# Performance work log

Measured on AMD Instinct MI355X. Metric: run time of the kernel, lower is better.

## Reference

```python
import jax, jax.numpy as jnp
import numpy as np

D_MODEL = 768
H = 6
DQK = 128
DV = 256
SCALE_BASE = 512.0


def _xpos(x, sign):
    """xPos rotary: x (B,T,H,d); sign=+1 for queries, -1 for keys."""
    B, T, Hn, d = x.shape
    half = d // 2
    pos = jnp.arange(T, dtype=jnp.float32)
    inv_freq = 1.0 / (10000.0 ** (jnp.arange(half, dtype=jnp.float32) / half))
    angles = pos[:, None] * inv_freq[None, :]                    # (T, half)
    zeta = (jnp.arange(half, dtype=jnp.float32) + half) / d      # (half,)
    decay = zeta[None, :] ** (sign * pos[:, None] / SCALE_BASE)  # (T, half)
    cos_a = (jnp.cos(angles) * decay)[None, :, None, :]
    sin_a = (jnp.sin(angles) * decay)[None, :, None, :]
    x1, x2 = x[..., :half], x[..., half:]
    return jnp.concatenate([x1 * cos_a - x2 * sin_a,
                            x1 * sin_a + x2 * cos_a], axis=-1)


def _decay_mask(T):
    """(H,T,T) causal decay mask, row-normalized by sqrt(row_sum)."""
    gammas = jnp.array([1.0 - 2.0 ** (-(5 + h)) for h in range(H)], dtype=jnp.float32)
    i = jnp.arange(T, dtype=jnp.float32)
    diff = i[:, None] - i[None, :]
    causal = (diff >= 0).astype(jnp.float32)
    D = (gammas[:, None, None] ** jnp.clip(diff, 0.0)[None]) * causal[None]
    row = jnp.clip(jnp.sum(D, axis=-1, keepdims=True), 1e-6)
    return D / jnp.sqrt(row)


def setup_inputs() -> dict:
    key = jax.random.key(0)
    ks = jax.random.split(key, 6)
    B, T = 2, 2048

    def xavier(k, shape):
        lim = float(np.sqrt(6.0 / (shape[0] + shape[1])))
        return jax.random.uniform(k, shape, jnp.float32, -lim, lim)

    return {
        "x": jax.random.normal(ks[0], (B, T, D_MODEL), jnp.float32),
        "Wq": xavier(ks[1], (D_MODEL, H * DQK)),
        "Wk": xavier(ks[2], (D_MODEL, H * DQK)),
        "Wv": xavier(ks[3], (D_MODEL, H * DV)),
        "Wg": xavier(ks[4], (D_MODEL, H * DV)),
        "Wo": xavier(ks[5], (H * DV, D_MODEL)),
        "gn_weight": jnp.ones((H * DV,), jnp.float32),
        "gn_bias": jnp.zeros((H * DV,), jnp.float32),
    }


def reference(x, Wq, Wk, Wv, Wg, Wo, gn_weight, gn_bias):
    B, T, _ = x.shape
    Q = (x @ Wq).reshape(B, T, H, DQK)
    K = (x @ Wk).reshape(B, T, H, DQK)
    V = (x @ Wv).reshape(B, T, H, DV)
    Q = _xpos(Q, 1.0)
    K = _xpos(K, -1.0)
    # retention scores: QK^T * scale * per-head decay mask (no softmax)
    scores = jnp.einsum('bihd,bjhd->bhij', Q, K) * (DQK ** -0.5)
    scores = scores * _decay_mask(T)[None]
    out = jnp.einsum('bhij,bjhv->bihv', scores, V)   # (B,T,H,DV)
    concat = out.reshape(B, T, H * DV)
    # GroupNorm over (channels-in-group, time) per (batch, group), as torch GN on (B,C,T)
    g = concat.transpose(0, 2, 1).reshape(B, H, DV, T)
    mean = jnp.mean(g, axis=(2, 3), keepdims=True)
    var = jnp.var(g, axis=(2, 3), keepdims=True)
    g = (g - mean) / jnp.sqrt(var + 1e-5)
    g = g.reshape(B, H * DV, T) * gn_weight[None, :, None] + gn_bias[None, :, None]
    normed = g.transpose(0, 2, 1)                    # (B,T,H*DV)
    gate = jax.nn.silu(x @ Wg)
    return (normed * gate) @ Wo
```

## Files before the change

### kernel.cpp

```cpp
#include <hip/hip_runtime.h>

typedef unsigned short u16;
typedef unsigned int u32;
typedef __attribute__((ext_vector_type(8))) short short8;
typedef __attribute__((ext_vector_type(4))) float f32x4;

#define DEV static __device__ __forceinline__

DEV float bf2f(u16 u){ u32 i = ((u32)u)<<16; float f; __builtin_memcpy(&f,&i,4); return f; }
DEV u16 f2bf(float f){ u32 i; __builtin_memcpy(&i,&f,4); u32 r = i + 0x7FFFu + ((i>>16)&1u); return (u16)(r>>16); }

DEV void gld16(const void* gp, void* lp){
  __builtin_amdgcn_global_load_lds((const __attribute__((address_space(1))) void*)gp,
                                   (__attribute__((address_space(3))) void*)lp, 16, 0, 0);
}

DEV int bcol(int n, int wc, int ln){ return ((n&1)<<4) + ln + (wc<<5) + ((n>>1)<<6); }

__global__ void k_prep(const float* __restrict__ x,
                       const float* __restrict__ Wq, const float* __restrict__ Wk,
                       const float* __restrict__ Wv, const float* __restrict__ Wg,
                       const float* __restrict__ Wo,
                       u16* __restrict__ xb, u16* __restrict__ WT, u16* __restrict__ WoT,
                       float4* __restrict__ tab){
  __shared__ float tile[32][33];
  int i = blockIdx.x, tid = threadIdx.x;
  if (i < 3072){
    size_t base = ((size_t)i*256 + tid)*4;
    float4 v = *(const float4*)(x + base);
    ushort4 o; o.x=f2bf(v.x); o.y=f2bf(v.y); o.z=f2bf(v.z); o.w=f2bf(v.w);
    *(ushort4*)(xb + base) = o;
  } else if (i < 7680){
    int j = i - 3072;
    const float* src; u16* dst; int N, K, bx, by;
    if (j < 576)       { src=Wq; dst=WT;             N=768;  K=768;  bx=j%24; by=j/24; }
    else if (j < 1152) { int q=j-576;  src=Wk; dst=WT+768ull*768;  N=768;  K=768;  bx=q%24; by=q/24; }
    else if (j < 2304) { int q=j-1152; src=Wv; dst=WT+1536ull*768; N=1536; K=768;  bx=q%48; by=q/48; }
    else if (j < 3456) { int q=j-2304; src=Wg; dst=WT+3072ull*768; N=1536; K=768;  bx=q%48; by=q/48; }
    else               { int q=j-3456; src=Wo; dst=WoT;            N=768;  K=1536; bx=q%24; by=q/24; }
    int n0 = bx*32, k0 = by*32;
    int tx = tid&31, ty = tid>>5;
    #pragma unroll
    for (int q=0;q<4;++q)
      tile[ty + q*8][tx] = src[(size_t)(k0 + ty + q*8)*N + n0 + tx];
    __syncthreads();
    #pragma unroll
    for (int q=0;q<4;++q)
      dst[(size_t)(n0 + ty + q*8)*K + k0 + tx] = f2bf(tile[tx][ty + q*8]);
  } else {
    int idx = (i-7680)*256 + tid;
    int t = idx>>6, j = idx&63;
    float inv_freq = expf(-(float)j * (9.210340371976184f/64.f));
    float angle = (float)t * inv_freq;
    float zeta = (float)(j + 64) * (1.f/128.f);
    float decq = exp2f(log2f(zeta) * ((float)t*(1.f/512.f)));
    float deck = 1.f/decq;
    float sn, cs; sincosf(angle, &sn, &cs);
    float4 o; o.x = cs*decq; o.y = sn*decq; o.z = cs*deck; o.w = sn*deck;
    tab[idx] = o;
  }
}

__global__ void k_trans(const u16* __restrict__ Vraw, u16* __restrict__ VbTs,
                        const u16* __restrict__ Kr, u16* __restrict__ KbT){
  __shared__ u16 tile[32][33];
  int i = blockIdx.x, tid = threadIdx.x;
  int tx = tid&31, ty = tid>>5;
  if (i < 6144){
    int bh = i>>9, r = i&511;
    int t0 = (r&63)*32, v0 = (r>>6)*32;
    int b = bh/6, h = bh%6;
    float lg2g = log2f(1.f - exp2f(-(float)(5+h)));
    float dec = exp2f(lg2g * (float)(63 - ((t0 + tx) & 63)));
    #pragma unroll
    for (int q=0;q<4;++q)
      tile[ty+q*8][tx] = Vraw[(size_t)(b*2048 + t0 + ty + q*8)*1536 + h*256 + v0 + tx];
    __syncthreads();
    #pragma unroll
    for (int q=0;q<4;++q)
      VbTs[(size_t)(bh*256 + v0 + ty + q*8)*2048 + t0 + tx] = f2bf(bf2f(tile[tx][ty+q*8]) * dec);
  } else {
    int j = i - 6144;
    int bh = j>>8, r = j&255;
    int t0 = (r&63)*32, d0 = (r>>6)*32;
    int b = bh/6, h = bh%6;
    #pragma unroll
    for (int q=0;q<4;++q)
      tile[ty+q*8][tx] = Kr[(size_t)(b*2048 + t0 + ty + q*8)*768 + h*128 + d0 + tx];
    __syncthreads();
    #pragma unroll
    for (int q=0;q<4;++q)
      KbT[(size_t)(bh*128 + d0 + ty + q*8)*2048 + t0 + tx] = tile[tx][ty+q*8];
  }
}

template<int MODE, int BM>
__global__ __launch_bounds__(256)
void k_gemm(const u16* __restrict__ A, const u16* __restrict__ BT,
            int K, int N,
            u16* __restrict__ Qr, u16* __restrict__ Kr,
            u16* __restrict__ Vraw, u16* __restrict__ Gb,
            float* __restrict__ Out, const float4* __restrict__ tab)
{
  constexpr int MR = BM/32;
  __shared__ u16 smem[BM*64 + 128*64];
  const int tid = threadIdx.x;
  const int w = tid>>6, l = tid&63, g = l>>4, ln = l&15;
  const int wr = w>>1, wc = w&1;
  const int m0 = blockIdx.x*BM, n0 = blockIdx.y*128;
  const f32x4 fz = {0.f,0.f,0.f,0.f};
  f32x4 acc[MR][4];
  #pragma unroll
  for (int m=0;m<MR;++m)
    #pragma unroll
    for (int n=0;n<4;++n) acc[m][n] = fz;

  const int nk = K>>6;
  for (int kt=0; kt<nk; ++kt){
    const int k0 = kt<<6;
    #pragma unroll
    for (int i=0;i<BM/32;++i){
      int off = i*4096 + tid*16;
      int row = off>>7;
      int colb = (off&127) ^ ((row&7)<<4);
      gld16(A  + (size_t)(m0+row)*K + k0 + (colb>>1), (char*)smem + i*4096 + w*1024);
    }
    #pragma unroll
    for (int i=0;i<4;++i){
      int off = i*4096 + tid*16;
      int row = off>>7;
      int colb = (off&127) ^ ((row&7)<<4);
      gld16(BT + (size_t)(n0+row)*K + k0 + (colb>>1), (char*)smem + BM*128 + i*4096 + w*1024);
    }
    __syncthreads();
    #pragma unroll
    for (int kk=0;kk<2;++kk){
      short8 a[MR], b[4];
      #pragma unroll
      for (int m=0;m<MR;++m){
        int row = wr*(BM/2) + m*16 + ln;
        int byte = row*128 + ((kk*64 + g*16) ^ ((row&7)<<4));
        a[m] = *(const short8*)((const char*)smem + byte);
      }
      #pragma unroll
      for (int n=0;n<4;++n){
        int row = bcol(n, wc, ln);
        int byte = BM*128 + row*128 + ((kk*64 + g*16) ^ ((row&7)<<4));
        b[n] = *(const short8*)((const char*)smem + byte);
      }
      #pragma unroll
      for (int m=0;m<MR;++m)
        #pragma unroll
        for (int n=0;n<4;++n)
          acc[m][n] = __builtin_amdgcn_mfma_f32_16x16x32_bf16(a[m], b[n], acc[m][n], 0,0,0);
    }
    __syncthreads();
  }

  const int region = n0/768;
  if (MODE==0 && region<2){
    const int hloc = (n0 - region*768) >> 7;
    u16* dst = (region==0) ? Qr : Kr;
    #pragma unroll
    for (int m=0;m<MR;++m){
      #pragma unroll
      for (int n=0;n<4;++n){
        int d = bcol(n, wc, ln);
        int j = d & 63;
        #pragma unroll
        for (int r=0;r<4;++r){
          int row = wr*(BM/2) + m*16 + g*4 + r;
          size_t grow = (size_t)(m0 + row);
          float self = acc[m][n][r];
          float part = acc[m][n^2][r];
          float4 f = tab[(grow & 2047)*64 + j];
          float cs = (region==0) ? f.x : f.z;
          float sn = (region==0) ? f.y : f.w;
          float val = (n<2) ? (self*cs - part*sn) : (part*sn + self*cs);
          dst[grow*768 + hloc*128 + d] = f2bf(val);
        }
      }
    }
  } else {
    #pragma unroll
    for (int m=0;m<MR;++m){
      int grow0 = m0 + wr*(BM/2) + m*16 + g*4;
      #pragma unroll
      for (int n=0;n<4;++n){
        int c = n0 + bcol(n, wc, ln);
        #pragma unroll
        for (int r=0;r<4;++r){
          float v = acc[m][n][r];
          size_t grow = (size_t)(grow0 + r);
          if (MODE == 1){
            Out[grow*(size_t)N + c] = v;
          } else {
            if (region<4) Vraw[grow*1536 + (c-1536)] = f2bf(v);
            else { float sg = v/(1.f+__expf(-v)); Gb[grow*1536 + (c-3072)] = f2bf(sg); }
          }
        }
      }
    }
  }
}

__global__ __launch_bounds__(256)
void k_passA(const u16* __restrict__ VbTs, const u16* __restrict__ KbT, u16* __restrict__ Zb)
{
  __shared__ u16 Kt[128*64];
  __shared__ u16 Vt[256*64];
  const int tid = threadIdx.x, w = tid>>6, l = tid&63, g = l>>4, ln = l&15;
  const int c = blockIdx.x, bh = blockIdx.y;
  const f32x4 fz = {0.f,0.f,0.f,0.f};

  #pragma unroll
  for (int i=0;i<4;++i){
    int off = i*4096 + tid*16;
    int row = off>>7;
    int colb = (off&127) ^ ((row&7)<<4);
    gld16(KbT + (size_t)(bh*128 + row)*2048 + c*64 + (colb>>1), (char*)Kt + i*4096 + w*1024);
  }
  #pragma unroll
  for (int i=0;i<8;++i){
    int off = i*4096 + tid*16;
    int row = off>>7;
    int colb = (off&127) ^ ((row&7)<<4);
    gld16(VbTs + (size_t)(bh*256 + row)*2048 + c*64 + (colb>>1), (char*)Vt + i*4096 + w*1024);
  }
  __syncthreads();

  f32x4 acc[4][8];
  #pragma unroll
  for (int m=0;m<4;++m)
    #pragma unroll
    for (int n=0;n<8;++n) acc[m][n] = fz;

  #pragma unroll
  for (int kk=0;kk<2;++kk){
    short8 va[4], kb[8];
    #pragma unroll
    for (int m=0;m<4;++m){
      int vrow = w*64 + m*16 + ln;
      int byte = vrow*128 + ((kk*64 + g*16) ^ ((vrow&7)<<4));
      va[m] = *(const short8*)((const char*)Vt + byte);
    }
    #pragma unroll
    for (int n=0;n<8;++n){
      int krow = n*16 + ln;
      int byte = krow*128 + ((kk*64 + g*16) ^ ((krow&7)<<4));
      kb[n] = *(const short8*)((const char*)Kt + byte);
    }
    #pragma unroll
    for (int m=0;m<4;++m)
      #pragma unroll
      for (int n=0;n<8;++n)
        acc[m][n] = __builtin_amdgcn_mfma_f32_16x16x32_bf16(va[m], kb[n], acc[m][n], 0,0,0);
  }

  u16* z = Zb + (size_t)(c*12 + bh)*32768;
  #pragma unroll
  for (int m=0;m<4;++m)
    #pragma unroll
    for (int n=0;n<8;++n)
      #pragma unroll
      for (int r=0;r<4;++r){
        int v = w*64 + m*16 + g*4 + r;
        int d = n*16 + ln;
        z[v*128 + d] = f2bf(acc[m][n][r]);
      }
}

__global__ __launch_bounds__(256)
void k_scan(const u16* __restrict__ Zb, u16* __restrict__ States)
{
  int gid = blockIdx.x*256 + threadIdx.x;
  int bh = gid >> 13;
  int e0 = (gid & 8191) * 4;
  const int h = bh % 6;
  const float lg2g = log2f(1.f - exp2f(-(float)(5+h)));
  const float gl = exp2f(lg2g * 64.f);
  ushort4 z[31];
  #pragma unroll
  for (int c=0;c<31;++c)
    z[c] = *(const ushort4*)(Zb + (size_t)(c*12 + bh)*32768 + e0);
  {
    ushort4 o; o.x=0;o.y=0;o.z=0;o.w=0;
    *(ushort4*)(States + (size_t)bh*32768 + e0) = o;
  }
  float S0=0.f,S1=0.f,S2=0.f,S3=0.f;
  #pragma unroll
  for (int c=1;c<32;++c){
    ushort4 zz = z[c-1];
    S0 = gl*S0 + bf2f(zz.x); S1 = gl*S1 + bf2f(zz.y);
    S2 = gl*S2 + bf2f(zz.z); S3 = gl*S3 + bf2f(zz.w);
    ushort4 o; o.x=f2bf(S0); o.y=f2bf(S1); o.z=f2bf(S2); o.w=f2bf(S3);
    *(ushort4*)(States + (size_t)(c*12 + bh)*32768 + e0) = o;
  }
}

__global__ __launch_bounds__(256)
void k_passC(const u16* __restrict__ Qb, const u16* __restrict__ Kb,
             const u16* __restrict__ VbTs, const u16* __restrict__ States,
             u16* __restrict__ Ofb, float* __restrict__ partials)
{
  __shared__ u16 Ks[64*128];
  __shared__ u16 Vt[256*64];
  __shared__ float Ps[64*64];
  __shared__ float red[8];
  const int tid = threadIdx.x, w = tid>>6, l = tid&63, g = l>>4, ln = l&15;
  const int c = blockIdx.x, bh = blockIdx.y, b = bh/6, h = bh%6;
  const float omg = exp2f(-(float)(5+h));
  const float gamma = 1.f - omg;
  const float lg2g = log2f(gamma);
  const float scale = 0.08838834764831845f;
  const int q0 = c*64;
  const f32x4 fz = {0.f,0.f,0.f,0.f};

  short8 aq[4];
  {
    const size_t qrow = (size_t)(b*2048 + q0 + w*16 + ln)*768 + h*128;
    #pragma unroll
    for (int kk=0;kk<4;++kk) aq[kk] = *(const short8*)(Qb + qrow + kk*32 + g*8);
  }

  #pragma unroll
  for (int i=0;i<4;++i){
    int off = i*4096 + tid*16;
    int row = off>>8;
    int colb = (off&255) ^ ((row&7)<<4);
    gld16(Kb + (size_t)(b*2048 + q0 + row)*768 + h*128 + (colb>>1),
          (char*)Ks + i*4096 + w*1024);
  }
  #pragma unroll
  for (int i=0;i<8;++i){
    int off = i*4096 + tid*16;
    int row = off>>7;
    int colb = (off&127) ^ ((row&7)<<4);
    gld16(VbTs + (size_t)(bh*256 + row)*2048 + q0 + (colb>>1),
          (char*)Vt + i*4096 + w*1024);
  }
  __syncthreads();

  f32x4 sacc[4]; sacc[0]=fz; sacc[1]=fz; sacc[2]=fz; sacc[3]=fz;
  #pragma unroll
  for (int kk=0;kk<4;++kk){
    #pragma unroll
    for (int n=0;n<4;++n){
      int row = n*16 + ln;
      int byte = row*256 + ((kk*64 + g*16) ^ ((row&7)<<4));
      short8 bk = *(const short8*)((const char*)Ks + byte);
      sacc[n] = __builtin_amdgcn_mfma_f32_16x16x32_bf16(aq[kk], bk, sacc[n], 0,0,0);
    }
  }
  #pragma unroll
  for (int n=0;n<4;++n){
    int kj = n*16 + ln;
    #pragma unroll
    for (int r=0;r<4;++r){
      int a = w*16 + g*4 + r;
      float p = (a >= kj) ? sacc[n][r] : 0.f;
      int prow = w*16 + g*4 + r;
      int byte = prow*256 + ((((n*16+ln)*4)) ^ ((prow&7)<<4));
      *(float*)((char*)Ps + byte) = p;
    }
  }
  f32x4 acc[16];
  #pragma unroll
  for (int i=0;i<16;++i) acc[i] = fz;
  #pragma unroll
  for (int kk2=0;kk2<2;++kk2){
    int prow = w*16 + ln;
    int base = prow*256;
    int c0 = kk2*128 + g*32;
    int sw = (prow&7)<<4;
    f32x4 p0 = *(const f32x4*)((const char*)Ps + base + ((c0   )^sw));
    f32x4 p1 = *(const f32x4*)((const char*)Ps + base + ((c0+16)^sw));
    short8 ap;
    #pragma unroll
    for (int jj=0;jj<4;++jj){ ap[jj] = (short)f2bf(p0[jj]); ap[4+jj] = (short)f2bf(p1[jj]); }
    #pragma unroll
    for (int n2=0;n2<16;++n2){
      int vrow = n2*16 + ln;
      int byte = vrow*128 + ((kk2*64 + g*16) ^ ((vrow&7)<<4));
      short8 bv = *(const short8*)((const char*)Vt + byte);
      acc[n2] = __builtin_amdgcn_mfma_f32_16x16x32_bf16(ap, bv, acc[n2], 0,0,0);
    }
  }
  const float gi64 = exp2f(-64.f*lg2g);
  #pragma unroll
  for (int i=0;i<16;++i){ acc[i][0]*=gi64; acc[i][1]*=gi64; acc[i][2]*=gi64; acc[i][3]*=gi64; }
  const u16* st = States + (size_t)(c*12 + bh)*32768;
  #pragma unroll
  for (int kk=0;kk<4;++kk){
    #pragma unroll
    for (int n2=0;n2<16;++n2){
      short8 sb = *(const short8*)(st + (n2*16 + ln)*128 + kk*32 + g*8);
      acc[n2] = __builtin_amdgcn_mfma_f32_16x16x32_bf16(aq[kk], sb, acc[n2], 0,0,0);
    }
  }
  float rf[4];
  #pragma unroll
  for (int r=0;r<4;++r){
    int a = w*16 + g*4 + r;
    int qi = q0 + a;
    float rs = (1.f - exp2f(lg2g*(float)(qi+1))) / omg;
    rf[r] = scale * exp2f(lg2g*(float)(a+1)) * rsqrtf(fmaxf(rs, 1e-6f));
  }
  float lsum=0.f, lsq=0.f;
  #pragma unroll
  for (int n2=0;n2<16;++n2){
    #pragma unroll
    for (int r=0;r<4;++r){
      float v = acc[n2][r]*rf[r];
      Ofb[(size_t)(b*2048 + q0 + w*16 + g*4 + r)*1536 + h*256 + n2*16 + ln] = f2bf(v);
      lsum += v; lsq += v*v;
    }
  }
  #pragma unroll
  for (int o=32;o;o>>=1){ lsum += __shfl_xor(lsum,o,64); lsq += __shfl_xor(lsq,o,64); }
  if (l==0){ red[w*2]=lsum; red[w*2+1]=lsq; }
  __syncthreads();
  if (tid==0){
    partials[(c*12+bh)*2]   = red[0]+red[2]+red[4]+red[6];
    partials[(c*12+bh)*2+1] = red[1]+red[3]+red[5]+red[7];
  }
}

__global__ __launch_bounds__(64)
void k_redstats(const float* __restrict__ partials, float* __restrict__ stats){
  int bh = blockIdx.x, l = threadIdx.x;
  float s=0.f, q=0.f;
  if (l < 32){ s = partials[(l*12+bh)*2]; q = partials[(l*12+bh)*2+1]; }
  #pragma unroll
  for (int o=16;o;o>>=1){ s += __shfl_xor(s,o,64); q += __shfl_xor(q,o,64); }
  if (l==0){ stats[bh*2] = s; stats[bh*2+1] = q; }
}

__global__ void k_gatenorm(const u16* __restrict__ Ofb, const u16* __restrict__ Gb,
                           const float* __restrict__ gnw, const float* __restrict__ gnb,
                           const float* __restrict__ stats, u16* __restrict__ Yb){
  size_t base = ((size_t)blockIdx.x*256 + threadIdx.x)*8;
  int m = (int)(base/1536);
  int c = (int)(base%1536);
  int bh = (m>>11)*6 + (c>>8);
  const float Ninv = 1.f/524288.f;
  float mean = stats[bh*2]*Ninv;
  float var = stats[bh*2+1]*Ninv - mean*mean;
  float rstd = rsqrtf(var + 1e-5f);
  short8 ov = *(const short8*)(Ofb + base);
  short8 gv = *(const short8*)(Gb + base);
  short8 yo;
  #pragma unroll
  for (int jj=0;jj<8;++jj){
    float o = bf2f((u16)ov[jj]);
    float nv = (o-mean)*rstd*gnw[c+jj] + gnb[c+jj];
    yo[jj] = (short)f2bf(nv * bf2f((u16)gv[jj]));
  }
  *(short8*)(Yb + base) = yo;
}

extern "C" void kernel_launch(void* const* d_in, const int* in_sizes, int n_in,
                              void* d_out, int out_size, void* d_ws, size_t ws_size,
                              hipStream_t stream)
{
  const float* x   = (const float*)d_in[0];
  const float* Wq  = (const float*)d_in[1];
  const float* Wk  = (const float*)d_in[2];
  const float* Wv  = (const float*)d_in[3];
  const float* Wg  = (const float*)d_in[4];
  const float* Wo  = (const float*)d_in[5];
  const float* gnw = (const float*)d_in[6];
  const float* gnb = (const float*)d_in[7];
  float* out = (float*)d_out;

  char* ws = (char*)d_ws;
  u16*   xb     = (u16*)  (ws + 0);
  u16*   WT     = (u16*)  (ws + 6291456);
  u16*   Vraw   = (u16*)  (ws + 13369344);
  u16*   KbT    = (u16*)  (ws + 6291456);
  u16*   States = (u16*)  (ws + 0);
  u16*   Yb     = (u16*)  (ws + 0);
  u16*   Kr     = (u16*)  (ws + 25952256);
  u16*   Qr     = (u16*)  (ws + 32243712);
  u16*   Gb     = (u16*)  (ws + 38535168);
  u16*   WoT    = (u16*)  (ws + 51118080);
  u16*   VbTs   = (u16*)  (ws + 53477376);
  u16*   Zb     = (u16*)  (ws + 66060288);
  u16*   Ofb    = (u16*)  (ws + 66060288);
  float* partials = (float*)(ws + 91226112);
  float* stats  = (float*)(ws + 91230208);
  float4* tab   = (float4*)(ws + 95158272);

  k_prep<<<8192, 256, 0, stream>>>(x, Wq, Wk, Wv, Wg, Wo, xb, WT, WoT, tab);
  k_gemm<0,128><<<dim3(32,36), 256, 0, stream>>>(xb, WT, 768, 4608, Qr, Kr, Vraw, Gb,
                                                 (float*)nullptr, tab);
  k_trans<<<9216, 256, 0, stream>>>(Vraw, VbTs, Kr, KbT);
  k_passA<<<dim3(31,12), 256, 0, stream>>>(VbTs, KbT, Zb);
  k_scan<<<384, 256, 0, stream>>>(Zb, States);
  k_passC<<<dim3(32,12), 256, 0, stream>>>(Qr, Kr, VbTs, States, Ofb, partials);
  k_redstats<<<12, 64, 0, stream>>>(partials, stats);
  k_gatenorm<<<3072, 256, 0, stream>>>(Ofb, Gb, gnw, gnb, stats, Yb);
  k_gemm<1,64><<<dim3(64,6), 256, 0, stream>>>(Yb, WoT, 1536, 768,
                                            (u16*)nullptr,(u16*)nullptr,(u16*)nullptr,(u16*)nullptr,
                                            out, (float4*)nullptr);
}
```

Baseline: 159.3 us.

## Move xPos rotation out of QKV GEMM epilogue and fuse stat reduction into gatenorm

The xPos rotary step is taken out of the projection GEMM epilogue, which used a permuted column mapping, and moved into a separate elementwise kernel that rotates Q and K in place. The GEMM returns to a plain column layout with split A/B shared buffers. The separate GroupNorm stats reduction kernel is removed: each gatenorm block now reduces the per-head partials itself, with a grid indexed by (time, batch-head). This trades one extra pass over Q and K for a simpler GEMM epilogue and one fewer launch.

```diff
diff --git a/kernel.cpp b/kernel.cpp
--- a/kernel.cpp
+++ b/kernel.cpp
@@ -14,8 +14,6 @@
   __builtin_amdgcn_global_load_lds((const __attribute__((address_space(1))) void*)gp,
                                    (__attribute__((address_space(3))) void*)lp, 16, 0, 0);
 }
-
-DEV int bcol(int n, int wc, int ln){ return ((n&1)<<4) + ln + (wc<<5) + ((n>>1)<<6); }
 
 __global__ void k_prep(const float* __restrict__ x,
                        const float* __restrict__ Wq, const float* __restrict__ Wk,
@@ -61,6 +59,36 @@
   }
 }
 
+__global__ void k_xpos2(u16* __restrict__ Qr, u16* __restrict__ Kr, const float4* __restrict__ tab){
+  int idx = blockIdx.x*256 + threadIdx.x;
+  int jg = idx & 15;
+  int h  = (idx>>4) % 6;
+  int m  = (idx>>4) / 6;
+  int t  = m & 2047;
+  size_t base = (size_t)m*768 + h*128 + jg*4;
+  ushort4 q1 = *(const ushort4*)(Qr + base);
+  ushort4 q2 = *(const ushort4*)(Qr + base + 64);
+  ushort4 k1 = *(const ushort4*)(Kr + base);
+  ushort4 k2 = *(const ushort4*)(Kr + base + 64);
+  ushort4 oq1, oq2, ok1, ok2;
+  const float4* tb = tab + t*64 + jg*4;
+  #pragma unroll
+  for (int jj=0;jj<4;++jj){
+    float4 f = tb[jj];
+    float a, b2;
+    a = bf2f(((const u16*)&q1)[jj]); b2 = bf2f(((const u16*)&q2)[jj]);
+    ((u16*)&oq1)[jj] = f2bf(a*f.x - b2*f.y);
+    ((u16*)&oq2)[jj] = f2bf(a*f.y + b2*f.x);
+    a = bf2f(((const u16*)&k1)[jj]); b2 = bf2f(((const u16*)&k2)[jj]);
+    ((u16*)&ok1)[jj] = f2bf(a*f.z - b2*f.w);
+    ((u16*)&ok2)[jj] = f2bf(a*f.w + b2*f.z);
+  }
+  *(ushort4*)(Qr + base)      = oq1;
+  *(ushort4*)(Qr + base + 64) = oq2;
+  *(ushort4*)(Kr + base)      = ok1;
+  *(ushort4*)(Kr + base + 64) = ok2;
+}
+
 __global__ void k_trans(const u16* __restrict__ Vraw, u16* __restrict__ VbTs,
                         const u16* __restrict__ Kr, u16* __restrict__ KbT){
   __shared__ u16 tile[32][33];
@@ -100,10 +128,11 @@
             int K, int N,
             u16* __restrict__ Qr, u16* __restrict__ Kr,
             u16* __restrict__ Vraw, u16* __restrict__ Gb,
-            float* __restrict__ Out, const float4* __restrict__ tab)
+            float* __restrict__ Out)
 {
   constexpr int MR = BM/32;
-  __shared__ u16 smem[BM*64 + 128*64];
+  __shared__ u16 As[BM*64];
+  __shared__ u16 Bs[128*64];
   const int tid = threadIdx.x;
   const int w = tid>>6, l = tid&63, g = l>>4, ln = l&15;
   const int wr = w>>1, wc = w&1;
@@ -123,14 +152,14 @@
       int off = i*4096 + tid*16;
       int row = off>>7;
       int colb = (off&127) ^ ((row&7)<<4);
-      gld16(A  + (size_t)(m0+row)*K + k0 + (colb>>1), (char*)smem + i*4096 + w*1024);
+      gld16(A  + (size_t)(m0+row)*K + k0 + (colb>>1), (char*)As + i*4096 + w*1024);
     }
     #pragma unroll
     for (int i=0;i<4;++i){
       int off = i*4096 + tid*16;
       int row = off>>7;
       int colb = (off&127) ^ ((row&7)<<4);
-      gld16(BT + (size_t)(n0+row)*K + k0 + (colb>>1), (char*)smem + BM*128 + i*4096 + w*1024);
+      gld16(BT + (size_t)(n0+row)*K + k0 + (colb>>1), (char*)Bs + i*4096 + w*1024);
     }
     __syncthreads();
     #pragma unroll
@@ -140,13 +169,13 @@
       for (int m=0;m<MR;++m){
         int row = wr*(BM/2) + m*16 + ln;
         int byte = row*128 + ((kk*64 + g*16) ^ ((row&7)<<4));
-        a[m] = *(const short8*)((const char*)smem + byte);
+        a[m] = *(const short8*)((const char*)As + byte);
       }
       #pragma unroll
       for (int n=0;n<4;++n){
-        int row = bcol(n, wc, ln);
-        int byte = BM*128 + row*128 + ((kk*64 + g*16) ^ ((row&7)<<4));
-        b[n] = *(const short8*)((const char*)smem + byte);
+        int row = wc*64 + n*16 + ln;
+        int byte = row*128 + ((kk*64 + g*16) ^ ((row&7)<<4));
+        b[n] = *(const short8*)((const char*)Bs + byte);
       }
       #pragma unroll
       for (int m=0;m<MR;++m)
@@ -156,48 +185,24 @@
     }
     __syncthreads();
   }
-
   const int region = n0/768;
-  if (MODE==0 && region<2){
-    const int hloc = (n0 - region*768) >> 7;
-    u16* dst = (region==0) ? Qr : Kr;
-    #pragma unroll
-    for (int m=0;m<MR;++m){
+  #pragma unroll
+  for (int m=0;m<MR;++m){
+    int grow0 = m0 + wr*(BM/2) + m*16 + g*4;
+    #pragma unroll
+    for (int n=0;n<4;++n){
+      int c = n0 + wc*64 + n*16 + ln;
       #pragma unroll
-      for (int n=0;n<4;++n){
-        int d = bcol(n, wc, ln);
-        int j = d & 63;
-        #pragma unroll
-        for (int r=0;r<4;++r){
-          int row = wr*(BM/2) + m*16 + g*4 + r;
-          size_t grow = (size_t)(m0 + row);
-          float self = acc[m][n][r];
-          float part = acc[m][n^2][r];
-          float4 f = tab[(grow & 2047)*64 + j];
-          float cs = (region==0) ? f.x : f.z;
-          float sn = (region==0) ? f.y : f.w;
-          float val = (n<2) ? (self*cs - part*sn) : (part*sn + self*cs);
-          dst[grow*768 + hloc*128 + d] = f2bf(val);
-        }
-      }
-    }
-  } else {
-    #pragma unroll
-    for (int m=0;m<MR;++m){
-      int grow0 = m0 + wr*(BM/2) + m*16 + g*4;
-      #pragma unroll
-      for (int n=0;n<4;++n){
-        int c = n0 + bcol(n, wc, ln);
-        #pragma unroll
-        for (int r=0;r<4;++r){
-          float v = acc[m][n][r];
-          size_t grow = (size_t)(grow0 + r);
-          if (MODE == 1){
-            Out[grow*(size_t)N + c] = v;
-          } else {
-            if (region<4) Vraw[grow*1536 + (c-1536)] = f2bf(v);
-            else { float sg = v/(1.f+__expf(-v)); Gb[grow*1536 + (c-3072)] = f2bf(sg); }
-          }
+      for (int r=0;r<4;++r){
+        float v = acc[m][n][r];
+        size_t grow = (size_t)(grow0 + r);
+        if (MODE == 1){
+          Out[grow*(size_t)N + c] = v;
+        } else {
+          if (region==0)      Qr[grow*768 + c] = f2bf(v);
+          else if (region==1) Kr[grow*768 + (c-768)] = f2bf(v);
+          else if (region<4)  Vraw[grow*1536 + (c-1536)] = f2bf(v);
+          else { float sg = v/(1.f+__expf(-v)); Gb[grow*1536 + (c-3072)] = f2bf(sg); }
         }
       }
     }
@@ -426,34 +431,33 @@
   }
 }
 
-__global__ __launch_bounds__(64)
-void k_redstats(const float* __restrict__ partials, float* __restrict__ stats){
-  int bh = blockIdx.x, l = threadIdx.x;
+__global__ __launch_bounds__(256)
+void k_gatenorm(const u16* __restrict__ Ofb, const u16* __restrict__ Gb,
+                const float* __restrict__ gnw, const float* __restrict__ gnb,
+                const float* __restrict__ partials, u16* __restrict__ Yb){
+  const int bh = blockIdx.y, b = bh/6, h = bh%6;
+  const int tid = threadIdx.x, l = tid&63;
   float s=0.f, q=0.f;
   if (l < 32){ s = partials[(l*12+bh)*2]; q = partials[(l*12+bh)*2+1]; }
   #pragma unroll
   for (int o=16;o;o>>=1){ s += __shfl_xor(s,o,64); q += __shfl_xor(q,o,64); }
-  if (l==0){ stats[bh*2] = s; stats[bh*2+1] = q; }
-}
-
-__global__ void k_gatenorm(const u16* __restrict__ Ofb, const u16* __restrict__ Gb,
-                           const float* __restrict__ gnw, const float* __restrict__ gnb,
-                           const float* __restrict__ stats, u16* __restrict__ Yb){
-  size_t base = ((size_t)blockIdx.x*256 + threadIdx.x)*8;
-  int m = (int)(base/1536);
-  int c = (int)(base%1536);
-  int bh = (m>>11)*6 + (c>>8);
+  s = __shfl(s, 0, 64); q = __shfl(q, 0, 64);
   const float Ninv = 1.f/524288.f;
-  float mean = stats[bh*2]*Ninv;
-  float var = stats[bh*2+1]*Ninv - mean*mean;
+  float mean = s*Ninv;
+  float var = q*Ninv - mean*mean;
   float rstd = rsqrtf(var + 1e-5f);
+
+  int t = blockIdx.x*8 + (tid>>5);
+  int v0 = (tid&31)*8;
+  size_t base = (size_t)(b*2048 + t)*1536 + h*256 + v0;
+  int cidx = h*256 + v0;
   short8 ov = *(const short8*)(Ofb + base);
   short8 gv = *(const short8*)(Gb + base);
   short8 yo;
   #pragma unroll
   for (int jj=0;jj<8;++jj){
     float o = bf2f((u16)ov[jj]);
-    float nv = (o-mean)*rstd*gnw[c+jj] + gnb[c+jj];
+    float nv = (o-mean)*rstd*gnw[cidx+jj] + gnb[cidx+jj];
     yo[jj] = (short)f2bf(nv * bf2f((u16)gv[jj]));
   }
   *(short8*)(Yb + base) = yo;
@@ -488,19 +492,17 @@
   u16*   Zb     = (u16*)  (ws + 66060288);
   u16*   Ofb    = (u16*)  (ws + 66060288);
   float* partials = (float*)(ws + 91226112);
-  float* stats  = (float*)(ws + 91230208);
   float4* tab   = (float4*)(ws + 95158272);
 
   k_prep<<<8192, 256, 0, stream>>>(x, Wq, Wk, Wv, Wg, Wo, xb, WT, WoT, tab);
-  k_gemm<0,128><<<dim3(32,36), 256, 0, stream>>>(xb, WT, 768, 4608, Qr, Kr, Vraw, Gb,
-                                                 (float*)nullptr, tab);
+  k_gemm<0,128><<<dim3(32,36), 256, 0, stream>>>(xb, WT, 768, 4608, Qr, Kr, Vraw, Gb, (float*)nullptr);
+  k_xpos2<<<1536, 256, 0, stream>>>(Qr, Kr, tab);
   k_trans<<<9216, 256, 0, stream>>>(Vraw, VbTs, Kr, KbT);
   k_passA<<<dim3(31,12), 256, 0, stream>>>(VbTs, KbT, Zb);
   k_scan<<<384, 256, 0, stream>>>(Zb, States);
   k_passC<<<dim3(32,12), 256, 0, stream>>>(Qr, Kr, VbTs, States, Ofb, partials);
-  k_redstats<<<12, 64, 0, stream>>>(partials, stats);
-  k_gatenorm<<<3072, 256, 0, stream>>>(Ofb, Gb, gnw, gnb, stats, Yb);
+  k_gatenorm<<<dim3(256,12), 256, 0, stream>>>(Ofb, Gb, gnw, gnb, partials, Yb);
   k_gemm<1,64><<<dim3(64,6), 256, 0, stream>>>(Yb, WoT, 1536, 768,
                                             (u16*)nullptr,(u16*)nullptr,(u16*)nullptr,(u16*)nullptr,
-                                            out, (float4*)nullptr);
-}
+                                            out);
+}
```

Result: faster. 150.5 us (-5.5%).
